# Kernel optimization log

Hardware: AMD Instinct MI355X
Metric: run time of the kernel (lower is better)

Reference implementation:

```python
import jax, jax.numpy as jnp
import numpy as np

N = 100000      # nodes (PF candidates)
E = 1600000     # edges, avg degree 16
CONT = 6        # continuous features
H = 32          # hidden_dim
PDGS = [1, 2, 11, 13, 22, 130, 211]


def _p(k, shape):
    return jax.random.normal(k, shape, jnp.float32) * 0.1


def setup_inputs() -> dict:
    key = jax.random.key(0)
    ks = jax.random.split(key, 24)
    x_cont = jax.random.normal(ks[0], (N, CONT), jnp.float32)
    pdg = jnp.array(PDGS, jnp.int32)[jax.random.randint(ks[1], (N,), 0, 7)]
    sign = jax.random.randint(ks[2], (N,), 0, 2) * 2 - 1
    charge = jax.random.randint(ks[3], (N,), -1, 2)
    pv = jax.random.randint(ks[4], (N,), 0, 8)
    x_cat = jnp.stack([pdg * sign, charge, pv], axis=1).astype(jnp.int32)
    edge_index = jax.random.randint(ks[5], (2, E), 0, N, jnp.int32)
    batch = jnp.zeros((N,), jnp.int32)
    return {
        "x_cont": x_cont, "x_cat": x_cat, "edge_index": edge_index, "batch": batch,
        "W_cont": _p(ks[6], (CONT, H // 2)), "b_cont": jnp.zeros((H // 2,), jnp.float32),
        "T_chrg": _p(ks[7], (3, H // 4)), "T_pdg": _p(ks[8], (7, H // 4)), "T_pv": _p(ks[9], (8, H // 4)),
        "W_cat": _p(ks[10], (3 * H // 4, H // 2)), "b_cat": jnp.zeros((H // 2,), jnp.float32),
        "W_enc": _p(ks[11], (H, H)), "b_enc": jnp.zeros((H,), jnp.float32),
        "g_all": jnp.ones((H,), jnp.float32), "be_all": jnp.zeros((H,), jnp.float32),
        "W_msg": _p(ks[12], (2 * H, H)), "b_msg": jnp.zeros((H,), jnp.float32),
        "g_conv": jnp.ones((H,), jnp.float32), "be_conv": jnp.zeros((H,), jnp.float32),
        "W_out1": _p(ks[13], (H, H // 2)), "b_out1": jnp.zeros((H // 2,), jnp.float32),
        "W_out2": _p(ks[14], (H // 2, 1)), "b_out2": jnp.zeros((1,), jnp.float32),
    }


def _batchnorm(x, gamma, beta, eps=1e-5):
    # training-mode BatchNorm1d: biased batch stats over the node axis
    mu = jnp.mean(x, axis=0)
    var = jnp.mean(jnp.square(x - mu), axis=0)
    return (x - mu) * jax.lax.rsqrt(var + eps) * gamma + beta


def reference(x_cont, x_cat, edge_index, batch,
              W_cont, b_cont, T_chrg, T_pdg, T_pv, W_cat, b_cat,
              W_enc, b_enc, g_all, be_all, W_msg, b_msg, g_conv, be_conv,
              W_out1, b_out1, W_out2, b_out2):
    elu = jax.nn.elu
    emb_cont = elu(x_cont @ W_cont + b_cont)                      # [N, H/2]
    emb_chrg = T_chrg[x_cat[:, 1] + 1]                            # [N, H/4]
    emb_pv = T_pv[x_cat[:, 2]]                                    # [N, H/4]
    pdg_remap = jnp.abs(x_cat[:, 0])
    for i, pdgval in enumerate(PDGS):  # fixed small constant loop, as in original
        pdg_remap = jnp.where(pdg_remap == pdgval, jnp.int32(i), pdg_remap)
    emb_pdg = T_pdg[pdg_remap]                                    # [N, H/4]
    emb_cat = elu(jnp.concatenate([emb_chrg, emb_pdg, emb_pv], axis=1) @ W_cat + b_cat)
    emb = elu(jnp.concatenate([emb_cat, emb_cont], axis=1) @ W_enc + b_enc)
    emb = _batchnorm(emb, g_all, be_all)                          # [N, H]
    # EdgeConv: m_ij = nn([x_i, x_j - x_i]), aggregate by max over incoming edges
    src, dst = edge_index[0], edge_index[1]
    x_i = emb[dst]
    x_j = emb[src]
    msg = jnp.concatenate([x_i, x_j - x_i], axis=1) @ W_msg + b_msg   # [E, H]
    agg = jax.ops.segment_max(msg, dst, num_segments=N)
    agg = jnp.where(jnp.isfinite(agg), agg, 0.0)                  # nodes w/o in-edges -> 0
    emb = emb + _batchnorm(agg, g_conv, be_conv)
    out = elu(emb @ W_out1 + b_out1) @ W_out2 + b_out2            # [N, 1]
    return out.squeeze(-1)
```

## Files before the change

kernel.cpp:

```cpp
#include <hip/hip_runtime.h>
#include <hip/hip_bf16.h>

#define NN 100000
#define EE 1600000
#define NB_SCAN 391

#define NBUCK 782
#define CPAD  16
#define NCB   128
#define NPART 391
#define NE4   400000
#define BCAP  2560

typedef __hip_bfloat16 bf16_t;
typedef int int4v __attribute__((ext_vector_type(4)));
typedef float f4 __attribute__((ext_vector_type(4)));

#define PARB  600000
#define EMB   604480
#define PBUF  3804480
#define QBUF  7004480
#define ABUF  10204480
#define SOFF  13404480
#define CURS  (SOFF + 256)
#define BASEO (CURS + 12512)
#define ROWP  (BASEO + 1024)
#define SRCL  (ROWP + 100002)

#define O_WCONT 0
#define O_BCONT 96
#define O_TCHRG 112
#define O_TPDG  136
#define O_TPV   192
#define O_WCAT  256
#define O_BCAT  640
#define O_WENC  656
#define O_BENC  1680
#define O_GALL  1712
#define O_BEALL 1744
#define O_WMSG  1776
#define O_BMSG  3824
#define O_GCONV 3856
#define O_BECONV 3888
#define O_WOUT1 3920
#define O_BOUT1 4432
#define O_WOUT2 4448
#define O_BOUT2 4464
#define NPAR    4465

__device__ __forceinline__ float bf(unsigned short u) {
    return __uint_as_float(((unsigned)u) << 16);
}
__device__ __forceinline__ f4 elu4(f4 v) {
    f4 r;
    r.x = v.x > 0.0f ? v.x : expm1f(v.x);
    r.y = v.y > 0.0f ? v.y : expm1f(v.y);
    r.z = v.z > 0.0f ? v.z : expm1f(v.z);
    r.w = v.w > 0.0f ? v.w : expm1f(v.w);
    return r;
}
__device__ __forceinline__ f4 f4max(f4 a, f4 b) {
    f4 r;
    r.x = fmaxf(a.x, b.x); r.y = fmaxf(a.y, b.y);
    r.z = fmaxf(a.z, b.z); r.w = fmaxf(a.w, b.w);
    return r;
}

struct InitArgs {
    const void* p[19];
    const unsigned short* wdet;
    int*        flagw;
    float*      par;
    int*        curs;
    float*      stats;
};

__global__ __launch_bounds__(256) void k_init(InitArgs a)
{
    const int offs[20] = {O_WCONT,O_BCONT,O_TCHRG,O_TPDG,O_TPV,O_WCAT,O_BCAT,O_WENC,
                          O_BENC,O_GALL,O_BEALL,O_WMSG,O_BMSG,O_GCONV,O_BECONV,
                          O_WOUT1,O_BOUT1,O_WOUT2,O_BOUT2,NPAR};
    __shared__ int sflag;
    int b = blockIdx.x, tid = threadIdx.x;
    int g = b * 256 + tid;
    if (g < NBUCK * CPAD) a.curs[g] = 0;
    if (g < 128) a.stats[g] = 0.0f;
    if (b == 0) {
        if (tid == 0) sflag = 0;
        __syncthreads();
        int bad = 0;
        for (int i = tid; i < 1024; i += 256) {
            unsigned e = (a.wdet[i] >> 7) & 0xFFu;
            if (e >= 137u) bad = 1;
        }
        if (bad) atomicOr(&sflag, 1);
        __syncthreads();
        int f32 = sflag;
        if (tid == 0) *a.flagw = f32;
        for (int i = tid; i < NPAR; i += 256) {
            int t = 0;
            while (offs[t + 1] <= i) t++;
            int l = i - offs[t];
            const void* s = a.p[t];
            a.par[i] = f32 ? ((const float*)s)[l] : bf(((const unsigned short*)s)[l]);
        }
    }
}

__global__ __launch_bounds__(256, 1) void k_fusedA(
    const int* __restrict__ eidx, int* __restrict__ curs,
    const void* __restrict__ xc, const int* __restrict__ x_cat,
    const float* __restrict__ par, const int* __restrict__ flag,
    float* __restrict__ emb)
{
    __shared__ f4 sWc4[24];
    __shared__ f4 sbc4[4];
    __shared__ f4 sTc4[6], sTp4[14], sTv4[16];
    __shared__ f4 sWcat4[96];
    __shared__ f4 sbcat4[4];
    __shared__ f4 sWe4[256];
    __shared__ f4 sbe4[8];
    int tid = threadIdx.x;
    int b = blockIdx.x;

    if (b < NCB) {
        __shared__ int cnt[NBUCK];
        for (int i = tid; i < NBUCK; i += 256) cnt[i] = 0;
        __syncthreads();
        const int4v* dst4 = (const int4v*)(eidx + EE);
        int i0 = b * (NE4 / NCB);
        int i1 = i0 + (NE4 / NCB);
        for (int i = i0 + tid; i < i1; i += 256) {
            int4v d = __builtin_nontemporal_load(&dst4[i]);
            atomicAdd(&cnt[d.x >> 7], 1);
            atomicAdd(&cnt[d.y >> 7], 1);
            atomicAdd(&cnt[d.z >> 7], 1);
            atomicAdd(&cnt[d.w >> 7], 1);
        }
        __syncthreads();
        for (int i = tid; i < NBUCK; i += 256) {
            int c = cnt[i];
            if (c) atomicAdd(&curs[i * CPAD], c);
        }
        return;
    }

    {
        float* s;
        s=(float*)sWc4;   for(int i=tid;i<96;  i+=256) s[i]=par[O_WCONT+i];
        s=(float*)sbc4;   for(int i=tid;i<16;  i+=256) s[i]=par[O_BCONT+i];
        s=(float*)sTc4;   for(int i=tid;i<24;  i+=256) s[i]=par[O_TCHRG+i];
        s=(float*)sTp4;   for(int i=tid;i<56;  i+=256) s[i]=par[O_TPDG+i];
        s=(float*)sTv4;   for(int i=tid;i<64;  i+=256) s[i]=par[O_TPV+i];
        s=(float*)sWcat4; for(int i=tid;i<384; i+=256) s[i]=par[O_WCAT+i];
        s=(float*)sbcat4; for(int i=tid;i<16;  i+=256) s[i]=par[O_BCAT+i];
        s=(float*)sWe4;   for(int i=tid;i<1024;i+=256) s[i]=par[O_WENC+i];
        s=(float*)sbe4;   for(int i=tid;i<32;  i+=256) s[i]=par[O_BENC+i];
    }
    __syncthreads();

    int n = (b - NCB) * 256 + tid;
    if (n >= NN) return;

    float x0,x1,x2,x3,x4,x5;
    if (*flag) {
        const float* xr = (const float*)xc + (size_t)n * 6;
        x0=xr[0]; x1=xr[1]; x2=xr[2]; x3=xr[3]; x4=xr[4]; x5=xr[5];
    } else {
        const unsigned* xr = (const unsigned*)xc + (size_t)n * 3;
        unsigned w0=xr[0], w1=xr[1], w2=xr[2];
        x0=__uint_as_float(w0<<16); x1=__uint_as_float(w0 & 0xFFFF0000u);
        x2=__uint_as_float(w1<<16); x3=__uint_as_float(w1 & 0xFFFF0000u);
        x4=__uint_as_float(w2<<16); x5=__uint_as_float(w2 & 0xFFFF0000u);
    }

    f4 ec[4];
    #pragma unroll
    for (int g = 0; g < 4; g++) {
        f4 a = sbc4[g];
        a += x0 * sWc4[0*4+g]; a += x1 * sWc4[1*4+g]; a += x2 * sWc4[2*4+g];
        a += x3 * sWc4[3*4+g]; a += x4 * sWc4[4*4+g]; a += x5 * sWc4[5*4+g];
        ec[g] = elu4(a);
    }

    int c0 = x_cat[n*3+0], c1 = x_cat[n*3+1], c2 = x_cat[n*3+2];
    int a0 = c0 < 0 ? -c0 : c0;
    int pi = (a0==1)?0:(a0==2)?1:(a0==11)?2:(a0==13)?3:(a0==22)?4:(a0==130)?5:6;
    int ci = c1 + 1;

    f4 t0a = sTc4[ci*2],  t0b = sTc4[ci*2+1];
    f4 t1a = sTp4[pi*2],  t1b = sTp4[pi*2+1];
    f4 t2a = sTv4[c2*2],  t2b = sTv4[c2*2+1];

    f4 ecat[4];
    #pragma unroll
    for (int g = 0; g < 4; g++) {
        f4 a = sbcat4[g];
        #pragma unroll
        for (int k = 0; k < 4; k++) a += t0a[k] * sWcat4[(k     )*4+g];
        #pragma unroll
        for (int k = 0; k < 4; k++) a += t0b[k] * sWcat4[(4 + k )*4+g];
        #pragma unroll
        for (int k = 0; k < 4; k++) a += t1a[k] * sWcat4[(8 + k )*4+g];
        #pragma unroll
        for (int k = 0; k < 4; k++) a += t1b[k] * sWcat4[(12 + k)*4+g];
        #pragma unroll
        for (int k = 0; k < 4; k++) a += t2a[k] * sWcat4[(16 + k)*4+g];
        #pragma unroll
        for (int k = 0; k < 4; k++) a += t2b[k] * sWcat4[(20 + k)*4+g];
        ecat[g] = elu4(a);
    }

    f4* o = (f4*)(emb + (size_t)n * 32);
    #pragma unroll
    for (int cg = 0; cg < 8; cg++) {
        f4 a = sbe4[cg];
        #pragma unroll
        for (int kg = 0; kg < 4; kg++) {
            #pragma unroll
            for (int k = 0; k < 4; k++)
                a += ecat[kg][k] * sWe4[(kg*4+k)*8 + cg];
        }
        #pragma unroll
        for (int kg = 0; kg < 4; kg++) {
            #pragma unroll
            for (int k = 0; k < 4; k++)
                a += ec[kg][k] * sWe4[(16 + kg*4+k)*8 + cg];
        }
        o[cg] = elu4(a);
    }
}

__global__ __launch_bounds__(1024) void k_scan782(int* __restrict__ curs,
                                                  int* __restrict__ base,
                                                  int* __restrict__ rowp)
{
    __shared__ int s[1024];
    int tid = threadIdx.x;
    int v = (tid < NBUCK) ? curs[tid * CPAD] : 0;
    s[tid] = v;
    __syncthreads();
    for (int off = 1; off < 1024; off <<= 1) {
        int x = (tid >= off) ? s[tid - off] : 0;
        __syncthreads();
        s[tid] += x;
        __syncthreads();
    }
    if (tid < NBUCK) {
        int bexc = s[tid] - v;
        base[tid] = bexc;
        curs[tid * CPAD] = bexc;
    }
    if (tid == NBUCK - 1) base[NBUCK] = s[tid];
    if (tid == 0) rowp[NN] = EE;
}

__global__ __launch_bounds__(256, 1) void k_partition(
    const int* __restrict__ eidx, int* __restrict__ curs, int* __restrict__ pe)
{
    __shared__ int cnt[NBUCK];
    __shared__ int start[NBUCK];
    int tid = threadIdx.x;
    int b = blockIdx.x;
    for (int i = tid; i < NBUCK; i += 256) cnt[i] = 0;
    __syncthreads();

    const int4v* src4 = (const int4v*)eidx;
    const int4v* dst4 = (const int4v*)(eidx + EE);
    int i0 = b << 10;
    int i1 = i0 + 1024; if (i1 > NE4) i1 = NE4;

    for (int i = i0 + tid; i < i1; i += 256) {
        int4v d = dst4[i];
        atomicAdd(&cnt[d.x >> 7], 1);
        atomicAdd(&cnt[d.y >> 7], 1);
        atomicAdd(&cnt[d.z >> 7], 1);
        atomicAdd(&cnt[d.w >> 7], 1);
    }
    __syncthreads();
    for (int i = tid; i < NBUCK; i += 256) {
        int c = cnt[i];
        start[i] = c ? atomicAdd(&curs[i * CPAD], c) : 0;
    }
    __syncthreads();
    for (int i = tid; i < NBUCK; i += 256) cnt[i] = 0;
    __syncthreads();
    for (int i = i0 + tid; i < i1; i += 256) {
        int4v s = src4[i];
        int4v d = dst4[i];
        int bk, r;
        bk = d.x >> 7; r = atomicAdd(&cnt[bk], 1); pe[start[bk] + r] = (s.x << 7) | (d.x & 127);
        bk = d.y >> 7; r = atomicAdd(&cnt[bk], 1); pe[start[bk] + r] = (s.y << 7) | (d.y & 127);
        bk = d.z >> 7; r = atomicAdd(&cnt[bk], 1); pe[start[bk] + r] = (s.z << 7) | (d.z & 127);
        bk = d.w >> 7; r = atomicAdd(&cnt[bk], 1); pe[start[bk] + r] = (s.w << 7) | (d.w & 127);
    }
}

__global__ __launch_bounds__(256) void k_fusedB(
    const int* __restrict__ cbase, const int* __restrict__ pe,
    int* __restrict__ rowp, int* __restrict__ srcl,
    const float* __restrict__ emb, float* __restrict__ stats)
{
    __shared__ int stage[BCAP];
    __shared__ int cnt[128], sc[128], ex[128];
    __shared__ float ls[64];
    int tid = threadIdx.x;
    int b = blockIdx.x;
    if (b < NBUCK) {
        int beg = cbase[b], end = cbase[b + 1];
        int m = end - beg;
        if (tid < 128) cnt[tid] = 0;
        __syncthreads();
        for (int i = tid; i < m; i += 256) {
            int p = pe[beg + i];
            if (i < BCAP) stage[i] = p;
            atomicAdd(&cnt[p & 127], 1);
        }
        __syncthreads();
        if (tid < 128) sc[tid] = cnt[tid];
        __syncthreads();
        for (int off = 1; off < 128; off <<= 1) {
            int x = (tid >= off && tid < 128) ? sc[tid - off] : 0;
            __syncthreads();
            if (tid < 128) sc[tid] += x;
            __syncthreads();
        }
        if (tid < 128) {
            int e0 = sc[tid] - cnt[tid];
            ex[tid] = e0;
            int node = b * 128 + tid;
            if (node < NN) rowp[node] = beg + e0;
            cnt[tid] = 0;
        }
        __syncthreads();
        for (int i = tid; i < m; i += 256) {
            int p = (i < BCAP) ? stage[i] : pe[beg + i];
            int dl = p & 127;
            int r = atomicAdd(&cnt[dl], 1);
            srcl[beg + ex[dl] + r] = p >> 7;
        }
        return;
    }
    if (tid < 64) ls[tid] = 0.0f;
    __syncthreads();
    int sb = b - NBUCK;
    int idx = sb * 256 + tid;
    int stride = 512 * 256;
    int c = idx & 31;
    float sum = 0.0f, q = 0.0f;
    for (int i = idx; i < NN * 32; i += stride) {
        float v = emb[i];
        sum += v; q += v * v;
    }
    sum += __shfl_xor(sum, 32);
    q   += __shfl_xor(q, 32);
    if ((tid & 63) < 32) {
        atomicAdd(&ls[c], sum);
        atomicAdd(&ls[32 + c], q);
    }
    __syncthreads();
    if (tid < 64) atomicAdd(&stats[tid], ls[tid]);
}

__global__ __launch_bounds__(256, 1) void k_fusedC(
    const float* __restrict__ par, const float* __restrict__ stats,
    const float* __restrict__ emb, float* __restrict__ P, float* __restrict__ Q)
{
    __shared__ f4 sWP4[256], sWQ4[256];
    __shared__ f4 sbP4[8], sbQ4[8];
    __shared__ float ssc[32], ssh[32];
    int tid = threadIdx.x;
    int b = blockIdx.x;
    if (tid < 32) {
        float mu  = stats[tid] * (1.0f / NN);
        float var = stats[32 + tid] * (1.0f / NN) - mu * mu;
        float s   = par[O_GALL + tid] * rsqrtf(var + 1e-5f);
        ssc[tid] = s;
        ssh[tid] = par[O_BEALL + tid] - mu * s;
    }
    __syncthreads();
    {
        float* wp = (float*)sWP4;
        float* wq = (float*)sWQ4;
        for (int e = tid; e < 1024; e += 256) {
            int k = e >> 5;
            float w1 = par[O_WMSG + e];
            float w2 = par[O_WMSG + 1024 + e];
            wp[e] = ssc[k] * (w1 - w2);
            wq[e] = ssc[k] * w2;
        }
    }
    if (tid < 32) {
        float aP = par[O_BMSG + tid], aQ = 0.0f;
        for (int k = 0; k < 32; k++) {
            float w1 = par[O_WMSG + k*32 + tid];
            float w2 = par[O_WMSG + (k+32)*32 + tid];
            aP += ssh[k] * (w1 - w2);
            aQ += ssh[k] * w2;
        }
        ((float*)sbP4)[tid] = aP;
        ((float*)sbQ4)[tid] = aQ;
    }
    __syncthreads();

    int n = b * 256 + tid;
    if (n >= NN) return;

    const f4* er = (const f4*)(emb + (size_t)n * 32);
    f4 e[8];
    #pragma unroll
    for (int g = 0; g < 8; g++) e[g] = er[g];

    f4* pr = (f4*)(P + (size_t)n * 32);
    f4* qr = (f4*)(Q + (size_t)n * 32);
    #pragma unroll
    for (int cg = 0; cg < 8; cg++) {
        f4 aP = sbP4[cg];
        f4 aQ = sbQ4[cg];
        #pragma unroll
        for (int kg = 0; kg < 8; kg++) {
            #pragma unroll
            for (int k = 0; k < 4; k++) {
                float ek = e[kg][k];
                aP += ek * sWP4[(kg*4+k)*8 + cg];
                aQ += ek * sWQ4[(kg*4+k)*8 + cg];
            }
        }
        pr[cg] = aP;
        qr[cg] = aQ;
    }
}

__global__ __launch_bounds__(256) void k_gather(
    const int* __restrict__ rowp, const int* __restrict__ srcl,
    const float* __restrict__ Q, const float* __restrict__ P,
    float* __restrict__ agg)
{
    int tid = threadIdx.x;
    int lane = tid & 63;
    int wave = tid >> 6;
    int n = blockIdx.x * 4 + wave;
    int slice = lane >> 3;
    int cg    = lane & 7;
    int beg = rowp[n], end = rowp[n + 1];
    const f4* Q4 = (const f4*)Q;

    f4 pv = (f4){0.f, 0.f, 0.f, 0.f};
    if (lane < 8 && end > beg) pv = ((const f4*)P)[(size_t)n * 8 + lane];

    f4 m = {-INFINITY, -INFINITY, -INFINITY, -INFINITY};
    for (int e = beg + slice; e < end; e += 32) {
        int e1 = min(e + 8,  end - 1);
        int e2 = min(e + 16, end - 1);
        int e3 = min(e + 24, end - 1);
        int s0 = __builtin_nontemporal_load(&srcl[e]);
        int s1 = __builtin_nontemporal_load(&srcl[e1]);
        int s2 = __builtin_nontemporal_load(&srcl[e2]);
        int s3 = __builtin_nontemporal_load(&srcl[e3]);
        f4 q0 = Q4[(size_t)s0 * 8 + cg];
        f4 q1 = Q4[(size_t)s1 * 8 + cg];
        f4 q2 = Q4[(size_t)s2 * 8 + cg];
        f4 q3 = Q4[(size_t)s3 * 8 + cg];
        q0 = f4max(q0, q1);
        q2 = f4max(q2, q3);
        m = f4max(m, f4max(q0, q2));
    }
    #pragma unroll
    for (int off = 8; off < 64; off <<= 1) {
        m.x = fmaxf(m.x, __shfl_xor(m.x, off));
        m.y = fmaxf(m.y, __shfl_xor(m.y, off));
        m.z = fmaxf(m.z, __shfl_xor(m.z, off));
        m.w = fmaxf(m.w, __shfl_xor(m.w, off));
    }
    if (lane < 8) {
        f4 o;
        if (end > beg) o = m + pv;
        else           o = (f4){0.f, 0.f, 0.f, 0.f};
        ((f4*)agg)[(size_t)n * 8 + lane] = o;
    }
}

__global__ __launch_bounds__(256) void k_stats(const float* __restrict__ xin,
                                               float* __restrict__ outsums, int count)
{
    __shared__ float ls[64];
    int tid = threadIdx.x;
    if (tid < 64) ls[tid] = 0.0f;
    __syncthreads();
    int idx = blockIdx.x * 256 + tid;
    int stride = gridDim.x * 256;
    int c = idx & 31;
    float s = 0.0f, q = 0.0f;
    for (int i = idx; i < count; i += stride) {
        float v = xin[i];
        s += v; q += v * v;
    }
    s += __shfl_xor(s, 32);
    q += __shfl_xor(q, 32);
    if ((tid & 63) < 32) {
        atomicAdd(&ls[c], s);
        atomicAdd(&ls[32 + c], q);
    }
    __syncthreads();
    if (tid < 64) atomicAdd(&outsums[tid], ls[tid]);
}

__global__ __launch_bounds__(256, 1) void k_out(
    const float* __restrict__ emb, const float* __restrict__ agg,
    const float* __restrict__ par, const float* __restrict__ stats,
    const int* __restrict__ flag, void* __restrict__ out)
{
    __shared__ f4 sW14[128];
    __shared__ f4 sb14[4], sW24[4];
    __shared__ f4 sc14[8], sh14[8], sc24[8], sh24[8];
    __shared__ float sb2s;
    int tid = threadIdx.x;
    {
        float* s = (float*)sW14;
        for (int i = tid; i < 512; i += 256) s[i] = par[O_WOUT1 + i];
    }
    if (tid < 16) {
        ((float*)sb14)[tid] = par[O_BOUT1 + tid];
        ((float*)sW24)[tid] = par[O_WOUT2 + tid];
    }
    if (tid < 32) {
        float mu  = stats[tid] * (1.0f / NN);
        float var = stats[32 + tid] * (1.0f / NN) - mu * mu;
        float s   = par[O_GALL + tid] * rsqrtf(var + 1e-5f);
        ((float*)sc14)[tid] = s;
        ((float*)sh14)[tid] = par[O_BEALL + tid] - mu * s;
        float mu2  = stats[64 + tid] * (1.0f / NN);
        float var2 = stats[96 + tid] * (1.0f / NN) - mu2 * mu2;
        float s2   = par[O_GCONV + tid] * rsqrtf(var2 + 1e-5f);
        ((float*)sc24)[tid] = s2;
        ((float*)sh24)[tid] = par[O_BECONV + tid] - mu2 * s2;
    }
    if (tid == 0) sb2s = par[O_BOUT2];
    __syncthreads();

    int n = blockIdx.x * 256 + tid;
    if (n >= NN) return;

    const f4* er = (const f4*)(emb + (size_t)n * 32);
    const f4* ar = (const f4*)(agg + (size_t)n * 32);
    f4 h[8];
    #pragma unroll
    for (int g = 0; g < 8; g++) {
        f4 ev = er[g];
        f4 av = ar[g];
        h[g] = ev * sc14[g] + sh14[g] + av * sc24[g] + sh24[g];
    }
    f4 o1[4];
    #pragma unroll
    for (int g = 0; g < 4; g++) {
        f4 acc = sb14[g];
        #pragma unroll
        for (int kg = 0; kg < 8; kg++) {
            #pragma unroll
            for (int k = 0; k < 4; k++)
                acc += h[kg][k] * sW14[(kg*4+k)*4 + g];
        }
        o1[g] = elu4(acc);
    }
    float acc = sb2s;
    #pragma unroll
    for (int g = 0; g < 4; g++) {
        f4 p = o1[g] * sW24[g];
        acc += p.x + p.y + p.z + p.w;
    }

    if (*flag) ((float*)out)[n] = acc;
    else       ((bf16_t*)out)[n] = __float2bfloat16(acc);
}

extern "C" void kernel_launch(void* const* d_in, const int* in_sizes, int n_in,
                              void* d_out, int out_size, void* d_ws, size_t ws_size,
                              hipStream_t stream)
{
    const void* x_cont = d_in[0];
    const int* x_cat = (const int*)d_in[1];
    const int* eidx  = (const int*)d_in[2];

    float* ws    = (float*)d_ws;
    float* par   = ws + PARB;
    float* emb   = ws + EMB;
    float* P     = ws + PBUF;
    float* Q     = ws + QBUF;
    float* agg   = ws + ABUF;
    int*   pe    = (int*)(ws + ABUF);
    float* stats = ws + SOFF;
    int*   flag  = (int*)(stats + 128);
    int*   curs  = (int*)(ws + CURS);
    int*   base  = (int*)(ws + BASEO);
    int*   rowp  = (int*)(ws + ROWP);
    int*   srcl  = (int*)(ws + SRCL);

    InitArgs ia;
    for (int t = 0; t < 19; t++) ia.p[t] = d_in[4 + t];
    ia.wdet = (const unsigned short*)d_in[11];
    ia.flagw = flag; ia.par = par; ia.curs = curs; ia.stats = stats;
    k_init<<<NB_SCAN, 256, 0, stream>>>(ia);

    k_fusedA<<<NCB + NB_SCAN, 256, 0, stream>>>(eidx, curs, x_cont, x_cat,
                                                par, flag, emb);
    k_scan782<<<1, 1024, 0, stream>>>(curs, base, rowp);
    k_partition<<<NPART, 256, 0, stream>>>(eidx, curs, pe);
    k_fusedB<<<NBUCK + 512, 256, 0, stream>>>(base, pe, rowp, srcl, emb, stats);
    k_fusedC<<<NB_SCAN, 256, 0, stream>>>(par, stats, emb, P, Q);
    k_gather<<<NN / 4, 256, 0, stream>>>(rowp, srcl, Q, P, agg);
    k_stats<<<512, 256, 0, stream>>>(agg, stats + 64, NN * 32);
    k_out<<<NB_SCAN, 256, 0, stream>>>(emb, agg, par, stats, flag, d_out);
}
```

Measured before the change: 294.5 us.

## Fuse pipeline into single cooperative persistent kernel with grid syncs

Adds a cooperative mega-kernel that runs every stage (param conversion, embedding, bucket counting, scan, BN stats, partition, P/Q projection, CSR build, max-gather and output MLP) inside one launch. Stages are separated by grid-wide syncs, and the conv BN statistics are folded into the gather loop. The aim is to remove the per-launch gaps and the separate stats pass. In exchange it pays for grid barriers, is limited to the occupancy-bounded grid size, and keeps the multi-kernel path as a fallback if cooperative launch is unavailable or fails.

```diff
diff --git a/kernel.cpp b/kernel.cpp
--- a/kernel.cpp
+++ b/kernel.cpp
@@ -1,5 +1,8 @@
 #include <hip/hip_runtime.h>
 #include <hip/hip_bf16.h>
+#include <hip/hip_cooperative_groups.h>
+
+namespace cg = cooperative_groups;
 
 #define NN 100000
 #define EE 1600000
@@ -66,6 +69,487 @@
     return r;
 }
 
+
+struct MegaArgs {
+    const void* p[19];
+    const unsigned short* wdet;
+    const int* eidx;
+    const void* xc;
+    const int* xcat;
+    float* par;
+    int*   flagw;
+    int*   curs;
+    float* stats;
+    int*   base;
+    int*   rowp;
+    int*   srcl;
+    int*   pe;
+    float* emb;
+    float* P;
+    float* Q;
+    float* agg;
+    void*  out;
+};
+
+struct SMemEmb { float wc[96], bc[16], tc[24], tp[56], tv[64], wcat[384], bcat[16], we[1024], be[32]; };
+struct SMemScan { int t[256]; };
+struct SMemPart { int cnt[NBUCK]; int start[NBUCK]; };
+struct SMemCsr  { int stage[BCAP]; int cnt[128]; int sc[128]; int ex[128]; };
+struct SMemPq   { float wp[1024], wq[1024], bp[32], bq[32], ssc[32], ssh[32]; };
+struct SMemSt   { float ls[64]; };
+struct SMemOut  { float w1[512], b1[16], w2[16], sc1[32], sh1[32], sc2[32], sh2[32], b2s; };
+union SMemU {
+    SMemEmb  emb;
+    SMemScan scan;
+    int      cnt782[NBUCK];
+    SMemPart part;
+    SMemCsr  csr;
+    SMemPq   pq;
+    SMemSt   st;
+    SMemOut  outp;
+};
+
+__global__ __launch_bounds__(256, 4) void k_mega(MegaArgs a)
+{
+    __shared__ alignas(16) SMemU sm;
+    cg::grid_group gg = cg::this_grid();
+    const int tid = threadIdx.x;
+    const int b   = blockIdx.x;
+    const int G   = gridDim.x;
+
+    {
+        int g = b * 256 + tid;
+        for (int i = g; i < NBUCK * CPAD; i += G * 256) a.curs[i] = 0;
+        if (g < 128) a.stats[g] = 0.0f;
+        if (b == 0) {
+            const int offs[20] = {O_WCONT,O_BCONT,O_TCHRG,O_TPDG,O_TPV,O_WCAT,O_BCAT,O_WENC,
+                                  O_BENC,O_GALL,O_BEALL,O_WMSG,O_BMSG,O_GCONV,O_BECONV,
+                                  O_WOUT1,O_BOUT1,O_WOUT2,O_BOUT2,NPAR};
+            if (tid == 0) sm.scan.t[0] = 0;
+            __syncthreads();
+            int bad = 0;
+            for (int i = tid; i < 1024; i += 256) {
+                unsigned e = (a.wdet[i] >> 7) & 0xFFu;
+                if (e >= 137u) bad = 1;
+            }
+            if (bad) atomicOr(&sm.scan.t[0], 1);
+            __syncthreads();
+            int f32 = sm.scan.t[0];
+            if (tid == 0) *a.flagw = f32;
+            for (int i = tid; i < NPAR; i += 256) {
+                int t = 0;
+                while (offs[t + 1] <= i) t++;
+                int l = i - offs[t];
+                const void* s = a.p[t];
+                a.par[i] = f32 ? ((const float*)s)[l] : bf(((const unsigned short*)s)[l]);
+            }
+        }
+    }
+    gg.sync();
+
+    if (b < NB_SCAN) {
+        const float* par = a.par;
+        float* s;
+        s=sm.emb.wc;   for(int i=tid;i<96;  i+=256) s[i]=par[O_WCONT+i];
+        s=sm.emb.bc;   for(int i=tid;i<16;  i+=256) s[i]=par[O_BCONT+i];
+        s=sm.emb.tc;   for(int i=tid;i<24;  i+=256) s[i]=par[O_TCHRG+i];
+        s=sm.emb.tp;   for(int i=tid;i<56;  i+=256) s[i]=par[O_TPDG+i];
+        s=sm.emb.tv;   for(int i=tid;i<64;  i+=256) s[i]=par[O_TPV+i];
+        s=sm.emb.wcat; for(int i=tid;i<384; i+=256) s[i]=par[O_WCAT+i];
+        s=sm.emb.bcat; for(int i=tid;i<16;  i+=256) s[i]=par[O_BCAT+i];
+        s=sm.emb.we;   for(int i=tid;i<1024;i+=256) s[i]=par[O_WENC+i];
+        s=sm.emb.be;   for(int i=tid;i<32;  i+=256) s[i]=par[O_BENC+i];
+        __syncthreads();
+
+        int n = b * 256 + tid;
+        if (n < NN) {
+            f4* sWc4 = (f4*)sm.emb.wc;  f4* sbc4 = (f4*)sm.emb.bc;
+            f4* sTc4 = (f4*)sm.emb.tc;  f4* sTp4 = (f4*)sm.emb.tp;  f4* sTv4 = (f4*)sm.emb.tv;
+            f4* sWcat4 = (f4*)sm.emb.wcat; f4* sbcat4 = (f4*)sm.emb.bcat;
+            f4* sWe4 = (f4*)sm.emb.we;  f4* sbe4 = (f4*)sm.emb.be;
+
+            float x0,x1,x2,x3,x4,x5;
+            if (*a.flagw) {
+                const float* xr = (const float*)a.xc + (size_t)n * 6;
+                x0=xr[0]; x1=xr[1]; x2=xr[2]; x3=xr[3]; x4=xr[4]; x5=xr[5];
+            } else {
+                const unsigned* xr = (const unsigned*)a.xc + (size_t)n * 3;
+                unsigned w0=xr[0], w1=xr[1], w2=xr[2];
+                x0=__uint_as_float(w0<<16); x1=__uint_as_float(w0 & 0xFFFF0000u);
+                x2=__uint_as_float(w1<<16); x3=__uint_as_float(w1 & 0xFFFF0000u);
+                x4=__uint_as_float(w2<<16); x5=__uint_as_float(w2 & 0xFFFF0000u);
+            }
+
+            f4 ec[4];
+            #pragma unroll
+            for (int g = 0; g < 4; g++) {
+                f4 acc = sbc4[g];
+                acc += x0 * sWc4[0*4+g]; acc += x1 * sWc4[1*4+g]; acc += x2 * sWc4[2*4+g];
+                acc += x3 * sWc4[3*4+g]; acc += x4 * sWc4[4*4+g]; acc += x5 * sWc4[5*4+g];
+                ec[g] = elu4(acc);
+            }
+
+            int c0 = a.xcat[n*3+0], c1 = a.xcat[n*3+1], c2 = a.xcat[n*3+2];
+            int a0 = c0 < 0 ? -c0 : c0;
+            int pi = (a0==1)?0:(a0==2)?1:(a0==11)?2:(a0==13)?3:(a0==22)?4:(a0==130)?5:6;
+            int ci = c1 + 1;
+
+            f4 t0a = sTc4[ci*2],  t0b = sTc4[ci*2+1];
+            f4 t1a = sTp4[pi*2],  t1b = sTp4[pi*2+1];
+            f4 t2a = sTv4[c2*2],  t2b = sTv4[c2*2+1];
+
+            f4 ecat[4];
+            #pragma unroll
+            for (int g = 0; g < 4; g++) {
+                f4 acc = sbcat4[g];
+                #pragma unroll
+                for (int k = 0; k < 4; k++) acc += t0a[k] * sWcat4[(k     )*4+g];
+                #pragma unroll
+                for (int k = 0; k < 4; k++) acc += t0b[k] * sWcat4[(4 + k )*4+g];
+                #pragma unroll
+                for (int k = 0; k < 4; k++) acc += t1a[k] * sWcat4[(8 + k )*4+g];
+                #pragma unroll
+                for (int k = 0; k < 4; k++) acc += t1b[k] * sWcat4[(12 + k)*4+g];
+                #pragma unroll
+                for (int k = 0; k < 4; k++) acc += t2a[k] * sWcat4[(16 + k)*4+g];
+                #pragma unroll
+                for (int k = 0; k < 4; k++) acc += t2b[k] * sWcat4[(20 + k)*4+g];
+                ecat[g] = elu4(acc);
+            }
+
+            f4* o = (f4*)(a.emb + (size_t)n * 32);
+            #pragma unroll
+            for (int cg2 = 0; cg2 < 8; cg2++) {
+                f4 acc = sbe4[cg2];
+                #pragma unroll
+                for (int kg = 0; kg < 4; kg++) {
+                    #pragma unroll
+                    for (int k = 0; k < 4; k++)
+                        acc += ecat[kg][k] * sWe4[(kg*4+k)*8 + cg2];
+                }
+                #pragma unroll
+                for (int kg = 0; kg < 4; kg++) {
+                    #pragma unroll
+                    for (int k = 0; k < 4; k++)
+                        acc += ec[kg][k] * sWe4[(16 + kg*4+k)*8 + cg2];
+                }
+                o[cg2] = elu4(acc);
+            }
+        }
+    } else if (b < NB_SCAN + NCB) {
+        for (int i = tid; i < NBUCK; i += 256) sm.cnt782[i] = 0;
+        __syncthreads();
+        int c = b - NB_SCAN;
+        const int4v* dst4 = (const int4v*)(a.eidx + EE);
+        int i0 = c * (NE4 / NCB);
+        int i1 = i0 + (NE4 / NCB);
+        for (int i = i0 + tid; i < i1; i += 256) {
+            int4v d = __builtin_nontemporal_load(&dst4[i]);
+            atomicAdd(&sm.cnt782[d.x >> 7], 1);
+            atomicAdd(&sm.cnt782[d.y >> 7], 1);
+            atomicAdd(&sm.cnt782[d.z >> 7], 1);
+            atomicAdd(&sm.cnt782[d.w >> 7], 1);
+        }
+        __syncthreads();
+        for (int i = tid; i < NBUCK; i += 256) {
+            int c2 = sm.cnt782[i];
+            if (c2) atomicAdd(&a.curs[i * CPAD], c2);
+        }
+    }
+    gg.sync();
+
+    if (b == 0) {
+        int t4 = tid * 4;
+        int v0=0,v1=0,v2=0,v3=0;
+        if (t4   < NBUCK) v0 = a.curs[(t4  )*CPAD];
+        if (t4+1 < NBUCK) v1 = a.curs[(t4+1)*CPAD];
+        if (t4+2 < NBUCK) v2 = a.curs[(t4+2)*CPAD];
+        if (t4+3 < NBUCK) v3 = a.curs[(t4+3)*CPAD];
+        sm.scan.t[tid] = v0+v1+v2+v3;
+        __syncthreads();
+        for (int off = 1; off < 256; off <<= 1) {
+            int x = (tid >= off) ? sm.scan.t[tid - off] : 0;
+            __syncthreads();
+            sm.scan.t[tid] += x;
+            __syncthreads();
+        }
+        int run = tid ? sm.scan.t[tid-1] : 0;
+        if (t4   < NBUCK) { a.base[t4  ] = run; a.curs[(t4  )*CPAD] = run; run += v0; }
+        if (t4+1 < NBUCK) { a.base[t4+1] = run; a.curs[(t4+1)*CPAD] = run; run += v1; }
+        if (t4+2 < NBUCK) { a.base[t4+2] = run; a.curs[(t4+2)*CPAD] = run; run += v2; }
+        if (t4+3 < NBUCK) { a.base[t4+3] = run; a.curs[(t4+3)*CPAD] = run; run += v3; }
+        if (tid == 255) a.base[NBUCK] = sm.scan.t[255];
+        if (tid == 0)   a.rowp[NN] = EE;
+    } else {
+        if (tid < 64) sm.st.ls[tid] = 0.0f;
+        __syncthreads();
+        int idx = (b - 1) * 256 + tid;
+        int stride = (G - 1) * 256;
+        int c = idx & 31;
+        float sum = 0.0f, q = 0.0f;
+        for (int i = idx; i < NN * 32; i += stride) {
+            float v = a.emb[i];
+            sum += v; q += v * v;
+        }
+        sum += __shfl_xor(sum, 32);
+        q   += __shfl_xor(q, 32);
+        if ((tid & 63) < 32) {
+            atomicAdd(&sm.st.ls[c], sum);
+            atomicAdd(&sm.st.ls[32 + c], q);
+        }
+        __syncthreads();
+        if (tid < 64) atomicAdd(&a.stats[tid], sm.st.ls[tid]);
+    }
+    gg.sync();
+
+    if (b < NPART) {
+        for (int i = tid; i < NBUCK; i += 256) sm.part.cnt[i] = 0;
+        __syncthreads();
+        const int4v* src4 = (const int4v*)a.eidx;
+        const int4v* dst4 = (const int4v*)(a.eidx + EE);
+        int i0 = b << 10;
+        int i1 = i0 + 1024; if (i1 > NE4) i1 = NE4;
+        for (int i = i0 + tid; i < i1; i += 256) {
+            int4v d = dst4[i];
+            atomicAdd(&sm.part.cnt[d.x >> 7], 1);
+            atomicAdd(&sm.part.cnt[d.y >> 7], 1);
+            atomicAdd(&sm.part.cnt[d.z >> 7], 1);
+            atomicAdd(&sm.part.cnt[d.w >> 7], 1);
+        }
+        __syncthreads();
+        for (int i = tid; i < NBUCK; i += 256) {
+            int c = sm.part.cnt[i];
+            sm.part.start[i] = c ? atomicAdd(&a.curs[i * CPAD], c) : 0;
+        }
+        __syncthreads();
+        for (int i = tid; i < NBUCK; i += 256) sm.part.cnt[i] = 0;
+        __syncthreads();
+        for (int i = i0 + tid; i < i1; i += 256) {
+            int4v s = src4[i];
+            int4v d = dst4[i];
+            int bk, r;
+            bk = d.x >> 7; r = atomicAdd(&sm.part.cnt[bk], 1); a.pe[sm.part.start[bk] + r] = (s.x << 7) | (d.x & 127);
+            bk = d.y >> 7; r = atomicAdd(&sm.part.cnt[bk], 1); a.pe[sm.part.start[bk] + r] = (s.y << 7) | (d.y & 127);
+            bk = d.z >> 7; r = atomicAdd(&sm.part.cnt[bk], 1); a.pe[sm.part.start[bk] + r] = (s.z << 7) | (d.z & 127);
+            bk = d.w >> 7; r = atomicAdd(&sm.part.cnt[bk], 1); a.pe[sm.part.start[bk] + r] = (s.w << 7) | (d.w & 127);
+        }
+    } else {
+        const float* par = a.par;
+        if (tid < 32) {
+            float mu  = a.stats[tid] * (1.0f / NN);
+            float var = a.stats[32 + tid] * (1.0f / NN) - mu * mu;
+            float sc  = par[O_GALL + tid] * rsqrtf(var + 1e-5f);
+            sm.pq.ssc[tid] = sc;
+            sm.pq.ssh[tid] = par[O_BEALL + tid] - mu * sc;
+        }
+        __syncthreads();
+        for (int e = tid; e < 1024; e += 256) {
+            int k = e >> 5;
+            float w1 = par[O_WMSG + e];
+            float w2 = par[O_WMSG + 1024 + e];
+            sm.pq.wp[e] = sm.pq.ssc[k] * (w1 - w2);
+            sm.pq.wq[e] = sm.pq.ssc[k] * w2;
+        }
+        if (tid < 32) {
+            float aP = par[O_BMSG + tid], aQ = 0.0f;
+            for (int k = 0; k < 32; k++) {
+                float w1 = par[O_WMSG + k*32 + tid];
+                float w2 = par[O_WMSG + (k+32)*32 + tid];
+                aP += sm.pq.ssh[k] * (w1 - w2);
+                aQ += sm.pq.ssh[k] * w2;
+            }
+            sm.pq.bp[tid] = aP;
+            sm.pq.bq[tid] = aQ;
+        }
+        __syncthreads();
+
+        int n = (b - NPART) * 256 + tid;
+        if (n < NN) {
+            f4* sWP4 = (f4*)sm.pq.wp; f4* sWQ4 = (f4*)sm.pq.wq;
+            f4* sbP4 = (f4*)sm.pq.bp; f4* sbQ4 = (f4*)sm.pq.bq;
+            const f4* er = (const f4*)(a.emb + (size_t)n * 32);
+            f4 e[8];
+            #pragma unroll
+            for (int g = 0; g < 8; g++) e[g] = er[g];
+            f4* pr = (f4*)(a.P + (size_t)n * 32);
+            f4* qr = (f4*)(a.Q + (size_t)n * 32);
+            #pragma unroll
+            for (int cg2 = 0; cg2 < 8; cg2++) {
+                f4 aP = sbP4[cg2];
+                f4 aQ = sbQ4[cg2];
+                #pragma unroll
+                for (int kg = 0; kg < 8; kg++) {
+                    #pragma unroll
+                    for (int k = 0; k < 4; k++) {
+                        float ek = e[kg][k];
+                        aP += ek * sWP4[(kg*4+k)*8 + cg2];
+                        aQ += ek * sWQ4[(kg*4+k)*8 + cg2];
+                    }
+                }
+                pr[cg2] = aP;
+                qr[cg2] = aQ;
+            }
+        }
+    }
+    gg.sync();
+
+    if (b < NBUCK) {
+        int beg = a.base[b], end = a.base[b + 1];
+        int m = end - beg;
+        if (tid < 128) sm.csr.cnt[tid] = 0;
+        __syncthreads();
+        for (int i = tid; i < m; i += 256) {
+            int p = a.pe[beg + i];
+            if (i < BCAP) sm.csr.stage[i] = p;
+            atomicAdd(&sm.csr.cnt[p & 127], 1);
+        }
+        __syncthreads();
+        if (tid < 128) sm.csr.sc[tid] = sm.csr.cnt[tid];
+        __syncthreads();
+        for (int off = 1; off < 128; off <<= 1) {
+            int x = (tid >= off && tid < 128) ? sm.csr.sc[tid - off] : 0;
+            __syncthreads();
+            if (tid < 128) sm.csr.sc[tid] += x;
+            __syncthreads();
+        }
+        if (tid < 128) {
+            int e0 = sm.csr.sc[tid] - sm.csr.cnt[tid];
+            sm.csr.ex[tid] = e0;
+            int node = b * 128 + tid;
+            if (node < NN) a.rowp[node] = beg + e0;
+            sm.csr.cnt[tid] = 0;
+        }
+        __syncthreads();
+        for (int i = tid; i < m; i += 256) {
+            int p = (i < BCAP) ? sm.csr.stage[i] : a.pe[beg + i];
+            int dl = p & 127;
+            int r = atomicAdd(&sm.csr.cnt[dl], 1);
+            a.srcl[beg + sm.csr.ex[dl] + r] = p >> 7;
+        }
+    }
+    gg.sync();
+
+    {
+        if (tid < 64) sm.st.ls[tid] = 0.0f;
+        __syncthreads();
+        int lane = tid & 63;
+        int wave = tid >> 6;
+        int w = b * 4 + wave;
+        int half  = lane >> 5;
+        int hl    = lane & 31;
+        int slice = hl >> 3;
+        int cg    = hl & 7;
+        const f4* Q4 = (const f4*)a.Q;
+        for (int n0 = w * 2; n0 < NN; n0 += G * 8) {
+            int n2 = n0 + half;
+            int beg = a.rowp[n2], end = a.rowp[n2 + 1];
+            f4 pv = (f4){0.f, 0.f, 0.f, 0.f};
+            if (hl < 8 && end > beg) pv = ((const f4*)a.P)[(size_t)n2 * 8 + hl];
+            f4 m = {-INFINITY, -INFINITY, -INFINITY, -INFINITY};
+            for (int e = beg + slice; e < end; e += 16) {
+                int e1 = min(e + 4,  end - 1);
+                int e2 = min(e + 8,  end - 1);
+                int e3 = min(e + 12, end - 1);
+                int s0 = __builtin_nontemporal_load(&a.srcl[e]);
+                int s1 = __builtin_nontemporal_load(&a.srcl[e1]);
+                int s2 = __builtin_nontemporal_load(&a.srcl[e2]);
+                int s3 = __builtin_nontemporal_load(&a.srcl[e3]);
+                f4 q0 = Q4[(size_t)s0 * 8 + cg];
+                f4 q1 = Q4[(size_t)s1 * 8 + cg];
+                f4 q2 = Q4[(size_t)s2 * 8 + cg];
+                f4 q3 = Q4[(size_t)s3 * 8 + cg];
+                q0 = f4max(q0, q1);
+                q2 = f4max(q2, q3);
+                m = f4max(m, f4max(q0, q2));
+            }
+            #pragma unroll
+            for (int off = 8; off < 32; off <<= 1) {
+                m.x = fmaxf(m.x, __shfl_xor(m.x, off));
+                m.y = fmaxf(m.y, __shfl_xor(m.y, off));
+                m.z = fmaxf(m.z, __shfl_xor(m.z, off));
+                m.w = fmaxf(m.w, __shfl_xor(m.w, off));
+            }
+            if (hl < 8) {
+                f4 o;
+                if (end > beg) o = m + pv;
+                else           o = (f4){0.f, 0.f, 0.f, 0.f};
+                ((f4*)a.agg)[(size_t)n2 * 8 + hl] = o;
+                atomicAdd(&sm.st.ls[hl*4+0], o.x);
+                atomicAdd(&sm.st.ls[hl*4+1], o.y);
+                atomicAdd(&sm.st.ls[hl*4+2], o.z);
+                atomicAdd(&sm.st.ls[hl*4+3], o.w);
+                atomicAdd(&sm.st.ls[32+hl*4+0], o.x*o.x);
+                atomicAdd(&sm.st.ls[32+hl*4+1], o.y*o.y);
+                atomicAdd(&sm.st.ls[32+hl*4+2], o.z*o.z);
+                atomicAdd(&sm.st.ls[32+hl*4+3], o.w*o.w);
+            }
+        }
+        __syncthreads();
+        if (tid < 64) atomicAdd(&a.stats[64 + tid], sm.st.ls[tid]);
+    }
+    gg.sync();
+
+    if (b < NB_SCAN) {
+        const float* par = a.par;
+        for (int i = tid; i < 512; i += 256) sm.outp.w1[i] = par[O_WOUT1 + i];
+        if (tid < 16) {
+            sm.outp.b1[tid] = par[O_BOUT1 + tid];
+            sm.outp.w2[tid] = par[O_WOUT2 + tid];
+        }
+        if (tid < 32) {
+            float mu  = a.stats[tid] * (1.0f / NN);
+            float var = a.stats[32 + tid] * (1.0f / NN) - mu * mu;
+            float sc  = par[O_GALL + tid] * rsqrtf(var + 1e-5f);
+            sm.outp.sc1[tid] = sc;
+            sm.outp.sh1[tid] = par[O_BEALL + tid] - mu * sc;
+            float mu2  = a.stats[64 + tid] * (1.0f / NN);
+            float var2 = a.stats[96 + tid] * (1.0f / NN) - mu2 * mu2;
+            float s2   = par[O_GCONV + tid] * rsqrtf(var2 + 1e-5f);
+            sm.outp.sc2[tid] = s2;
+            sm.outp.sh2[tid] = par[O_BECONV + tid] - mu2 * s2;
+        }
+        if (tid == 0) sm.outp.b2s = par[O_BOUT2];
+        __syncthreads();
+
+        int n = b * 256 + tid;
+        if (n < NN) {
+            f4* sW14 = (f4*)sm.outp.w1; f4* sb14 = (f4*)sm.outp.b1; f4* sW24 = (f4*)sm.outp.w2;
+            f4* sc14 = (f4*)sm.outp.sc1; f4* sh14 = (f4*)sm.outp.sh1;
+            f4* sc24 = (f4*)sm.outp.sc2; f4* sh24 = (f4*)sm.outp.sh2;
+            const f4* er = (const f4*)(a.emb + (size_t)n * 32);
+            const f4* ar = (const f4*)(a.agg + (size_t)n * 32);
+            f4 h[8];
+            #pragma unroll
+            for (int g = 0; g < 8; g++) {
+                f4 ev = er[g];
+                f4 av = ar[g];
+                h[g] = ev * sc14[g] + sh14[g] + av * sc24[g] + sh24[g];
+            }
+            f4 o1[4];
+            #pragma unroll
+            for (int g = 0; g < 4; g++) {
+                f4 acc = sb14[g];
+                #pragma unroll
+                for (int kg = 0; kg < 8; kg++) {
+                    #pragma unroll
+                    for (int k = 0; k < 4; k++)
+                        acc += h[kg][k] * sW14[(kg*4+k)*4 + g];
+                }
+                o1[g] = elu4(acc);
+            }
+            float acc = sm.outp.b2s;
+            #pragma unroll
+            for (int g = 0; g < 4; g++) {
+                f4 p = o1[g] * sW24[g];
+                acc += p.x + p.y + p.z + p.w;
+            }
+            if (*a.flagw) ((float*)a.out)[n] = acc;
+            else          ((bf16_t*)a.out)[n] = __float2bfloat16(acc);
+        }
+    }
+}
+
+
 struct InitArgs {
     const void* p[19];
     const unsigned short* wdet;
@@ -573,6 +1057,7 @@
     else       ((bf16_t*)out)[n] = __float2bfloat16(acc);
 }
 
+
 extern "C" void kernel_launch(void* const* d_in, const int* in_sizes, int n_in,
                               void* d_out, int out_size, void* d_ws, size_t ws_size,
                               hipStream_t stream)
@@ -595,6 +1080,37 @@
     int*   rowp  = (int*)(ws + ROWP);
     int*   srcl  = (int*)(ws + SRCL);
 
+    static int coop_state = -1;
+    if (coop_state == -1) {
+        int dev = 0;
+        hipGetDevice(&dev);
+        int coop = 0;
+        hipDeviceGetAttribute(&coop, hipDeviceAttributeCooperativeLaunch, dev);
+        int ncu = 0;
+        hipDeviceGetAttribute(&ncu, hipDeviceAttributeMultiprocessorCount, dev);
+        int nb = 0;
+        hipOccupancyMaxActiveBlocksPerMultiprocessor(&nb, k_mega, 256, 0);
+        int mg = ncu * nb;
+        if (mg > 1024) mg = 1024;
+        coop_state = (coop && mg >= 2 * NB_SCAN) ? mg : 0;
+    }
+
+    if (coop_state > 0) {
+        MegaArgs ma;
+        for (int t = 0; t < 19; t++) ma.p[t] = d_in[4 + t];
+        ma.wdet = (const unsigned short*)d_in[11];
+        ma.eidx = eidx; ma.xc = x_cont; ma.xcat = x_cat;
+        ma.par = par; ma.flagw = flag; ma.curs = curs; ma.stats = stats;
+        ma.base = base; ma.rowp = rowp; ma.srcl = srcl; ma.pe = pe;
+        ma.emb = emb; ma.P = P; ma.Q = Q; ma.agg = agg; ma.out = d_out;
+        void* kargs[] = { &ma };
+        hipError_t rc = hipLaunchCooperativeKernel((const void*)k_mega, dim3(coop_state),
+                                                   dim3(256), kargs, 0, stream);
+        if (rc == hipSuccess) return;
+        (void)hipGetLastError();
+        coop_state = 0;
+    }
+
     InitArgs ia;
     for (int t = 0; t < 19; t++) ia.p[t] = d_in[4 + t];
     ia.wdet = (const unsigned short*)d_in[11];
```

Result: no change. 291.8 us (-0.9%).
